# Kernel optimization log

Measured on AMD Instinct MI355X. Metric: run time of the kernel, lower is better.

The kernel has to match this reference:

```python
import jax, jax.numpy as jnp
import numpy as np

INPUT_SIZE = 2
HIDDEN = 128
OUTPUT = 2
FUTURE = 50


def setup_inputs() -> dict:
    key = jax.random.key(0)
    ks = jax.random.split(key, 7)
    B, T = 4096, 512
    s = 1.0 / np.sqrt(HIDDEN)
    x = jax.random.normal(ks[0], (B, T, INPUT_SIZE), dtype=jnp.float32)
    W_ih = jax.random.uniform(ks[1], (4 * HIDDEN, INPUT_SIZE), minval=-s, maxval=s, dtype=jnp.float32)
    W_hh = jax.random.uniform(ks[2], (4 * HIDDEN, HIDDEN), minval=-s, maxval=s, dtype=jnp.float32)
    b_ih = jax.random.uniform(ks[3], (4 * HIDDEN,), minval=-s, maxval=s, dtype=jnp.float32)
    b_hh = jax.random.uniform(ks[4], (4 * HIDDEN,), minval=-s, maxval=s, dtype=jnp.float32)
    fc_w = jax.random.uniform(ks[5], (OUTPUT, HIDDEN), minval=-s, maxval=s, dtype=jnp.float32)
    fc_b = jax.random.uniform(ks[6], (OUTPUT,), minval=-s, maxval=s, dtype=jnp.float32)
    return {"x": x, "W_ih": W_ih, "W_hh": W_hh, "b_ih": b_ih, "b_hh": b_hh, "fc_w": fc_w, "fc_b": fc_b}


def reference(x, W_ih, W_hh, b_ih, b_hh, fc_w, fc_b):
    B = x.shape[0]

    def cell(h, c, xt):
        # gates: [B, 4H], PyTorch LSTMCell order i, f, g, o
        gates = xt @ W_ih.T + b_ih + h @ W_hh.T + b_hh
        i, f, g, o = jnp.split(gates, 4, axis=-1)
        c_new = jax.nn.sigmoid(f) * c + jax.nn.sigmoid(i) * jnp.tanh(g)
        h_new = jax.nn.sigmoid(o) * jnp.tanh(c_new)
        return h_new, c_new

    h0 = jnp.zeros((B, HIDDEN), dtype=x.dtype)
    c0 = jnp.zeros((B, HIDDEN), dtype=x.dtype)

    def encode_step(carry, xt):
        h, c = carry
        h, c = cell(h, c, xt)
        return (h, c), None

    (h, c), _ = jax.lax.scan(encode_step, (h0, c0), jnp.swapaxes(x, 0, 1))

    def forecast_step(carry, _):
        h, c = carry
        y = h @ fc_w.T + fc_b  # [B, OUTPUT]
        h, c = cell(h, c, y)
        return (h, c), y

    (_, _), ys = jax.lax.scan(forecast_step, (h, c), None, length=FUTURE)
    # ys: [FUTURE, B, OUTPUT] -> torch.cat(outputs, dim=1) -> [B, FUTURE*OUTPUT]
    return jnp.swapaxes(ys, 0, 1).reshape(B, FUTURE * OUTPUT)
```

## Files before the change

### kernel.cpp

```cpp
#include <hip/hip_runtime.h>

#define HIDDEN 128
#define TSTEPS 512
#define NFUT 50
#define BR 16
#define THREADS 512
#define HPITCH 136

typedef __bf16 bf16x8 __attribute__((ext_vector_type(8)));
typedef float floatx4 __attribute__((ext_vector_type(4)));

union B8 { int4 i; bf16x8 v; };

#if defined(__has_builtin)
#  if __has_builtin(__builtin_amdgcn_exp2f)
#    define EXP2F(x) __builtin_amdgcn_exp2f(x)
#  else
#    define EXP2F(x) exp2f(x)
#  endif
#  if __has_builtin(__builtin_amdgcn_rcpf)
#    define RCPF(x) __builtin_amdgcn_rcpf(x)
#  else
#    define RCPF(x) (1.0f / (x))
#  endif
#else
#  define EXP2F(x) exp2f(x)
#  define RCPF(x) (1.0f / (x))
#endif

#define L2E  1.4426950408889634f
#define L2E2 2.8853900817779268f

__global__ __launch_bounds__(THREADS, 2)
void lstm_forecast_kernel(const float* __restrict__ x,
                          const float* __restrict__ W_ih,
                          const float* __restrict__ W_hh,
                          const float* __restrict__ b_ih,
                          const float* __restrict__ b_hh,
                          const float* __restrict__ fc_w,
                          const float* __restrict__ fc_b,
                          float* __restrict__ out) {
    __shared__ __align__(16) uint2  xa[TSTEPS * BR];
    __shared__ __align__(16) __bf16 h_lds[2][BR * HPITCH];
    __shared__ __align__(16) float  fcw_lds[2][HIDDEN];

    const int tid  = threadIdx.x;
    const int wave = tid >> 6;
    const int lane = tid & 63;
    const int quad = lane >> 4;
    const int l15  = lane & 15;
    const int rb   = blockIdx.x * BR;

    if (tid < 256) fcw_lds[tid >> 7][tid & 127] = fc_w[tid];

    {
        const int row = tid & 15;
        for (int tb = tid >> 4; tb < TSTEPS; tb += THREADS >> 4) {
            float2 xv = *(const float2*)&x[(size_t)(rb + row) * (2 * TSTEPS) + tb * 2];
            __bf16 x0h = (__bf16)xv.x, x1h = (__bf16)xv.y;
            __bf16 x0r = (__bf16)(xv.x - (float)x0h);
            __bf16 x1r = (__bf16)(xv.y - (float)x1h);
            uint2 d;
            d.x = (unsigned)__builtin_bit_cast(unsigned short, x0h) |
                  ((unsigned)__builtin_bit_cast(unsigned short, x1h) << 16);
            d.y = (unsigned)__builtin_bit_cast(unsigned short, x0r) |
                  ((unsigned)__builtin_bit_cast(unsigned short, x1r) << 16);
            xa[tb * BR + row] = d;
        }
    }
    for (int i = tid; i < BR * HPITCH; i += THREADS) h_lds[0][i] = (__bf16)0.0f;

    bf16x8 bfrag[4][4];
    B8 bfx[4];
    float wih0[4], wih1[4], bsum[4];
    const int u = wave * 16 + l15;
    const float fcb0 = fc_b[0], fcb1 = fc_b[1];
#pragma unroll
    for (int g = 0; g < 4; ++g) {
        const int cg = g * HIDDEN + u;
        wih0[g] = W_ih[cg * 2 + 0];
        wih1[g] = W_ih[cg * 2 + 1];
        bsum[g] = b_ih[cg] + b_hh[cg];
#pragma unroll
        for (int ks = 0; ks < 4; ++ks) {
            const float* wp = W_hh + (size_t)cg * HIDDEN + ks * 32 + quad * 8;
            bf16x8 bb;
#pragma unroll
            for (int j = 0; j < 8; ++j) bb[j] = (__bf16)wp[j];
            bfrag[g][ks] = bb;
        }
        B8 t; t.i = make_int4(0, 0, 0, 0);
        if (quad == 0) {
            __bf16 w0h = (__bf16)wih0[g], w1h = (__bf16)wih1[g];
            __bf16 w0l = (__bf16)(wih0[g] - (float)w0h);
            __bf16 w1l = (__bf16)(wih1[g] - (float)w1h);
            __bf16 bh  = (__bf16)bsum[g];
            __bf16 bl  = (__bf16)(bsum[g] - (float)bh);
            bf16x8 bv = {w0h, w1h, bh, bl, w0h, w1h, w0l, w1l};
            t.v = bv;
        }
        bfx[g] = t;
    }

    const unsigned qm    = (quad == 0) ? 0xFFFFFFFFu : 0u;
    const unsigned onesq = 0x3F803F80u & qm;

    float cst[4] = {0.f, 0.f, 0.f, 0.f};

    auto ew = [&](floatx4 a0, floatx4 a1, floatx4 a2, floatx4 a3, __bf16* hd) {
#pragma unroll
        for (int reg = 0; reg < 4; ++reg) {
            const float gi = a0[reg], gf = a1[reg], gg = a2[reg], go = a3[reg];
            const float ea = EXP2F(-L2E * gi);
            const float eb = EXP2F(-L2E2 * gg);
            const float R  = RCPF((1.f + ea) * (1.f + eb));
            const float ig = (1.f - eb) * R;
            const float sf = RCPF(1.f + EXP2F(-L2E * gf));
            const float cn = sf * cst[reg] + ig;
            cst[reg] = cn;
            const float cc = fmaxf(cn, -30.f);
            const float ed = EXP2F(-L2E2 * cc);
            const float eo = EXP2F(-L2E * go);
            const float R2 = RCPF((1.f + eo) * (1.f + ed));
            const float hn = (1.f - ed) * R2;
            hd[(quad * 4 + reg) * HPITCH + u] = (__bf16)hn;
        }
    };

    auto cellE = [&](const __bf16* hs, __bf16* hd, int t) {
        const uint2 xd = xa[t * BR + l15];
        B8 xf; xf.i = make_int4((int)(xd.x & qm), (int)onesq, (int)(xd.y & qm), (int)(xd.x & qm));
        bf16x8 af[4];
#pragma unroll
        for (int ks = 0; ks < 4; ++ks)
            af[ks] = *(const bf16x8*)&hs[l15 * HPITCH + ks * 32 + quad * 8];
        const floatx4 z = {0.f, 0.f, 0.f, 0.f};
        floatx4 acc[4];
#pragma unroll
        for (int g = 0; g < 4; ++g)
            acc[g] = __builtin_amdgcn_mfma_f32_16x16x32_bf16(xf.v, bfx[g].v, z, 0, 0, 0);
#pragma unroll
        for (int ks = 0; ks < 4; ++ks)
#pragma unroll
            for (int g = 0; g < 4; ++g)
                acc[g] = __builtin_amdgcn_mfma_f32_16x16x32_bf16(af[ks], bfrag[g][ks], acc[g], 0, 0, 0);
        ew(acc[0], acc[1], acc[2], acc[3], hd);
        __syncthreads();
    };

    __syncthreads();

    for (int t = 0; t < TSTEPS; t += 2) {
        cellE(h_lds[0], h_lds[1], t);
        cellE(h_lds[1], h_lds[0], t + 1);
    }

    float bs2[4];
#pragma unroll
    for (int g = 0; g < 4; ++g) {
        bs2[g] = bsum[g] + wih0[g] * fcb0 + wih1[g] * fcb1;
#pragma unroll
        for (int ks = 0; ks < 4; ++ks) {
            const int k0 = ks * 32 + quad * 8;
            bf16x8 bb = bfrag[g][ks];
#pragma unroll
            for (int j = 0; j < 8; ++j) {
                const float wv = (float)bb[j] + wih0[g] * fcw_lds[0][k0 + j]
                                             + wih1[g] * fcw_lds[1][k0 + j];
                bb[j] = (__bf16)wv;
            }
            bfrag[g][ks] = bb;
        }
    }

    auto cellF = [&](const __bf16* hs, __bf16* hd) {
        bf16x8 af[4];
#pragma unroll
        for (int ks = 0; ks < 4; ++ks)
            af[ks] = *(const bf16x8*)&hs[l15 * HPITCH + ks * 32 + quad * 8];
        floatx4 acc[4];
#pragma unroll
        for (int g = 0; g < 4; ++g)
            acc[g] = (floatx4){bs2[g], bs2[g], bs2[g], bs2[g]};
#pragma unroll
        for (int ks = 0; ks < 4; ++ks)
#pragma unroll
            for (int g = 0; g < 4; ++g)
                acc[g] = __builtin_amdgcn_mfma_f32_16x16x32_bf16(af[ks], bfrag[g][ks], acc[g], 0, 0, 0);
        ew(acc[0], acc[1], acc[2], acc[3], hd);
        __syncthreads();
    };

    auto emitY = [&](const __bf16* hs, int f) {
        if (wave == 0) {
            const int r = lane & 15, seg = lane >> 4;
            const __bf16* hp = &hs[r * HPITCH + seg * 32];
            float p0 = 0.f, p1 = 0.f;
#pragma unroll
            for (int js = 0; js < 4; ++js) {
                bf16x8 hv = *(const bf16x8*)&hp[js * 8];
                const float4* f0 = (const float4*)&fcw_lds[0][seg * 32 + js * 8];
                const float4* f1 = (const float4*)&fcw_lds[1][seg * 32 + js * 8];
                float4 a0 = f0[0], b0 = f0[1], a1 = f1[0], b1 = f1[1];
                p0 += (float)hv[0]*a0.x + (float)hv[1]*a0.y + (float)hv[2]*a0.z + (float)hv[3]*a0.w
                    + (float)hv[4]*b0.x + (float)hv[5]*b0.y + (float)hv[6]*b0.z + (float)hv[7]*b0.w;
                p1 += (float)hv[0]*a1.x + (float)hv[1]*a1.y + (float)hv[2]*a1.z + (float)hv[3]*a1.w
                    + (float)hv[4]*b1.x + (float)hv[5]*b1.y + (float)hv[6]*b1.z + (float)hv[7]*b1.w;
            }
            p0 += __shfl_xor(p0, 16); p0 += __shfl_xor(p0, 32);
            p1 += __shfl_xor(p1, 16); p1 += __shfl_xor(p1, 32);
            if (seg == 0) {
                float* op = &out[(size_t)(rb + r) * (2 * NFUT) + f * 2];
                op[0] = p0 + fcb0;
                op[1] = p1 + fcb1;
            }
        }
    };

    for (int f = 0; f < NFUT; f += 2) {
        emitY(h_lds[0], f);
        cellF(h_lds[0], h_lds[1]);
        emitY(h_lds[1], f + 1);
        cellF(h_lds[1], h_lds[0]);
    }
}

extern "C" void kernel_launch(void* const* d_in, const int* in_sizes, int n_in,
                              void* d_out, int out_size, void* d_ws, size_t ws_size,
                              hipStream_t stream) {
    const float* x    = (const float*)d_in[0];
    const float* W_ih = (const float*)d_in[1];
    const float* W_hh = (const float*)d_in[2];
    const float* b_ih = (const float*)d_in[3];
    const float* b_hh = (const float*)d_in[4];
    const float* fc_w = (const float*)d_in[5];
    const float* fc_b = (const float*)d_in[6];
    float* out = (float*)d_out;

    const int B = in_sizes[0] / (TSTEPS * 2);
    const int grid = B / BR;
    lstm_forecast_kernel<<<grid, THREADS, 0, stream>>>(x, W_ih, W_hh, b_ih, b_hh, fc_w, fc_b, out);
}
```

Measured before the change: 534.3 us.

## Split LSTM gate work across 16 waves with lane-shuffle gate exchange

```diff
diff --git a/kernel.cpp b/kernel.cpp
--- a/kernel.cpp
+++ b/kernel.cpp
@@ -4,7 +4,7 @@
 #define TSTEPS 512
 #define NFUT 50
 #define BR 16
-#define THREADS 512
+#define THREADS 1024
 #define HPITCH 136
 
 typedef __bf16 bf16x8 __attribute__((ext_vector_type(8)));
@@ -31,7 +31,7 @@
 #define L2E  1.4426950408889634f
 #define L2E2 2.8853900817779268f
 
-__global__ __launch_bounds__(THREADS, 2)
+__global__ __launch_bounds__(THREADS, 4)
 void lstm_forecast_kernel(const float* __restrict__ x,
                           const float* __restrict__ W_ih,
                           const float* __restrict__ W_hh,
@@ -49,6 +49,8 @@
     const int lane = tid & 63;
     const int quad = lane >> 4;
     const int l15  = lane & 15;
+    const int hi   = (l15 >> 3) & 1;
+    const int uu   = wave * 8 + (l15 & 7);
     const int rb   = blockIdx.x * BR;
 
     if (tid < 256) fcw_lds[tid >> 7][tid & 127] = fc_w[tid];
@@ -70,60 +72,70 @@
     }
     for (int i = tid; i < BR * HPITCH; i += THREADS) h_lds[0][i] = (__bf16)0.0f;
 
-    bf16x8 bfrag[4][4];
-    B8 bfx[4];
-    float wih0[4], wih1[4], bsum[4];
-    const int u = wave * 16 + l15;
+    bf16x8 bfrag[2][4];
+    B8 bfx[2];
+    float wih0[2], wih1[2], bsum[2];
     const float fcb0 = fc_b[0], fcb1 = fc_b[1];
 #pragma unroll
-    for (int g = 0; g < 4; ++g) {
-        const int cg = g * HIDDEN + u;
-        wih0[g] = W_ih[cg * 2 + 0];
-        wih1[g] = W_ih[cg * 2 + 1];
-        bsum[g] = b_ih[cg] + b_hh[cg];
+    for (int tt = 0; tt < 2; ++tt) {
+        const int g  = tt * 2 + hi;
+        const int cg = g * HIDDEN + uu;
+        wih0[tt] = W_ih[cg * 2 + 0];
+        wih1[tt] = W_ih[cg * 2 + 1];
+        bsum[tt] = b_ih[cg] + b_hh[cg];
 #pragma unroll
         for (int ks = 0; ks < 4; ++ks) {
             const float* wp = W_hh + (size_t)cg * HIDDEN + ks * 32 + quad * 8;
             bf16x8 bb;
 #pragma unroll
             for (int j = 0; j < 8; ++j) bb[j] = (__bf16)wp[j];
-            bfrag[g][ks] = bb;
+            bfrag[tt][ks] = bb;
         }
         B8 t; t.i = make_int4(0, 0, 0, 0);
         if (quad == 0) {
-            __bf16 w0h = (__bf16)wih0[g], w1h = (__bf16)wih1[g];
-            __bf16 w0l = (__bf16)(wih0[g] - (float)w0h);
-            __bf16 w1l = (__bf16)(wih1[g] - (float)w1h);
-            __bf16 bh  = (__bf16)bsum[g];
-            __bf16 bl  = (__bf16)(bsum[g] - (float)bh);
+            __bf16 w0h = (__bf16)wih0[tt], w1h = (__bf16)wih1[tt];
+            __bf16 w0l = (__bf16)(wih0[tt] - (float)w0h);
+            __bf16 w1l = (__bf16)(wih1[tt] - (float)w1h);
+            __bf16 bh  = (__bf16)bsum[tt];
+            __bf16 bl  = (__bf16)(bsum[tt] - (float)bh);
             bf16x8 bv = {w0h, w1h, bh, bl, w0h, w1h, w0l, w1l};
             t.v = bv;
         }
-        bfx[g] = t;
+        bfx[tt] = t;
     }
 
     const unsigned qm    = (quad == 0) ? 0xFFFFFFFFu : 0u;
     const unsigned onesq = 0x3F803F80u & qm;
 
-    float cst[4] = {0.f, 0.f, 0.f, 0.f};
-
-    auto ew = [&](floatx4 a0, floatx4 a1, floatx4 a2, floatx4 a3, __bf16* hd) {
-#pragma unroll
-        for (int reg = 0; reg < 4; ++reg) {
-            const float gi = a0[reg], gf = a1[reg], gg = a2[reg], go = a3[reg];
-            const float ea = EXP2F(-L2E * gi);
-            const float eb = EXP2F(-L2E2 * gg);
+    float cst[2] = {0.f, 0.f};
+
+    auto finish = [&](floatx4 a0, floatx4 a1, __bf16* hd) {
+        float s;
+        s = hi ? a0[0] : a0[2]; const float r1 = __shfl_xor(s, 8);
+        s = hi ? a0[1] : a0[3]; const float r2 = __shfl_xor(s, 8);
+        s = hi ? a1[0] : a1[2]; const float r3 = __shfl_xor(s, 8);
+        s = hi ? a1[1] : a1[3]; const float r4 = __shfl_xor(s, 8);
+        float gi[2], gf[2], gg[2], go[2];
+        gi[0] = hi ? r1 : a0[0];  gi[1] = hi ? r2 : a0[1];
+        gf[0] = hi ? a0[2] : r1;  gf[1] = hi ? a0[3] : r2;
+        gg[0] = hi ? r3 : a1[0];  gg[1] = hi ? r4 : a1[1];
+        go[0] = hi ? a1[2] : r3;  go[1] = hi ? a1[3] : r4;
+        const int rbase = quad * 4 + hi * 2;
+#pragma unroll
+        for (int j = 0; j < 2; ++j) {
+            const float ea = EXP2F(-L2E * gi[j]);
+            const float eb = EXP2F(-L2E2 * gg[j]);
             const float R  = RCPF((1.f + ea) * (1.f + eb));
             const float ig = (1.f - eb) * R;
-            const float sf = RCPF(1.f + EXP2F(-L2E * gf));
-            const float cn = sf * cst[reg] + ig;
-            cst[reg] = cn;
+            const float sf = RCPF(1.f + EXP2F(-L2E * gf[j]));
+            const float cn = sf * cst[j] + ig;
+            cst[j] = cn;
             const float cc = fmaxf(cn, -30.f);
             const float ed = EXP2F(-L2E2 * cc);
-            const float eo = EXP2F(-L2E * go);
+            const float eo = EXP2F(-L2E * go[j]);
             const float R2 = RCPF((1.f + eo) * (1.f + ed));
             const float hn = (1.f - ed) * R2;
-            hd[(quad * 4 + reg) * HPITCH + u] = (__bf16)hn;
+            hd[(rbase + j) * HPITCH + uu] = (__bf16)hn;
         }
     };
 
@@ -135,16 +147,14 @@
         for (int ks = 0; ks < 4; ++ks)
             af[ks] = *(const bf16x8*)&hs[l15 * HPITCH + ks * 32 + quad * 8];
         const floatx4 z = {0.f, 0.f, 0.f, 0.f};
-        floatx4 acc[4];
-#pragma unroll
-        for (int g = 0; g < 4; ++g)
-            acc[g] = __builtin_amdgcn_mfma_f32_16x16x32_bf16(xf.v, bfx[g].v, z, 0, 0, 0);
-#pragma unroll
-        for (int ks = 0; ks < 4; ++ks)
-#pragma unroll
-            for (int g = 0; g < 4; ++g)
-                acc[g] = __builtin_amdgcn_mfma_f32_16x16x32_bf16(af[ks], bfrag[g][ks], acc[g], 0, 0, 0);
-        ew(acc[0], acc[1], acc[2], acc[3], hd);
+        floatx4 acc0 = __builtin_amdgcn_mfma_f32_16x16x32_bf16(xf.v, bfx[0].v, z, 0, 0, 0);
+        floatx4 acc1 = __builtin_amdgcn_mfma_f32_16x16x32_bf16(xf.v, bfx[1].v, z, 0, 0, 0);
+#pragma unroll
+        for (int ks = 0; ks < 4; ++ks) {
+            acc0 = __builtin_amdgcn_mfma_f32_16x16x32_bf16(af[ks], bfrag[0][ks], acc0, 0, 0, 0);
+            acc1 = __builtin_amdgcn_mfma_f32_16x16x32_bf16(af[ks], bfrag[1][ks], acc1, 0, 0, 0);
+        }
+        finish(acc0, acc1, hd);
         __syncthreads();
     };
 
@@ -155,21 +165,21 @@
         cellE(h_lds[1], h_lds[0], t + 1);
     }
 
-    float bs2[4];
-#pragma unroll
-    for (int g = 0; g < 4; ++g) {
-        bs2[g] = bsum[g] + wih0[g] * fcb0 + wih1[g] * fcb1;
+    float bs2[2];
+#pragma unroll
+    for (int tt = 0; tt < 2; ++tt) {
+        bs2[tt] = bsum[tt] + wih0[tt] * fcb0 + wih1[tt] * fcb1;
 #pragma unroll
         for (int ks = 0; ks < 4; ++ks) {
             const int k0 = ks * 32 + quad * 8;
-            bf16x8 bb = bfrag[g][ks];
+            bf16x8 bb = bfrag[tt][ks];
 #pragma unroll
             for (int j = 0; j < 8; ++j) {
-                const float wv = (float)bb[j] + wih0[g] * fcw_lds[0][k0 + j]
-                                             + wih1[g] * fcw_lds[1][k0 + j];
+                const float wv = (float)bb[j] + wih0[tt] * fcw_lds[0][k0 + j]
+                                             + wih1[tt] * fcw_lds[1][k0 + j];
                 bb[j] = (__bf16)wv;
             }
-            bfrag[g][ks] = bb;
+            bfrag[tt][ks] = bb;
         }
     }
 
@@ -178,16 +188,14 @@
 #pragma unroll
         for (int ks = 0; ks < 4; ++ks)
             af[ks] = *(const bf16x8*)&hs[l15 * HPITCH + ks * 32 + quad * 8];
-        floatx4 acc[4];
-#pragma unroll
-        for (int g = 0; g < 4; ++g)
-            acc[g] = (floatx4){bs2[g], bs2[g], bs2[g], bs2[g]};
-#pragma unroll
-        for (int ks = 0; ks < 4; ++ks)
-#pragma unroll
-            for (int g = 0; g < 4; ++g)
-                acc[g] = __builtin_amdgcn_mfma_f32_16x16x32_bf16(af[ks], bfrag[g][ks], acc[g], 0, 0, 0);
-        ew(acc[0], acc[1], acc[2], acc[3], hd);
+        floatx4 acc0 = {bs2[0], bs2[0], bs2[0], bs2[0]};
+        floatx4 acc1 = {bs2[1], bs2[1], bs2[1], bs2[1]};
+#pragma unroll
+        for (int ks = 0; ks < 4; ++ks) {
+            acc0 = __builtin_amdgcn_mfma_f32_16x16x32_bf16(af[ks], bfrag[0][ks], acc0, 0, 0, 0);
+            acc1 = __builtin_amdgcn_mfma_f32_16x16x32_bf16(af[ks], bfrag[1][ks], acc1, 0, 0, 0);
+        }
+        finish(acc0, acc1, hd);
         __syncthreads();
     };
 
```

Result: slower. 594.2 us (+11.2%).
